# Performance work log

Measured on AMD Instinct MI355X. Metric: run time of the kernel, lower is better.

Reference implementation:

```python
import jax, jax.numpy as jnp
import numpy as np

D = 384      # n_embed_dims
H = 6        # n_heads
HS = D // H  # head_size = 64
T = 256      # block_size
B = 256
EPS = 1e-5


def setup_inputs() -> dict:
    key = jax.random.key(0)
    ks = jax.random.split(key, 12)
    s_in = 1.0 / np.sqrt(D)
    s_ff = 1.0 / np.sqrt(4 * D)
    return {
        "x": jax.random.normal(ks[0], (B, T, D), jnp.float32),
        # per-head QKV weights, stacked [H, D, HS] (Linear bias=False)
        "wq": jax.random.normal(ks[1], (H, D, HS), jnp.float32) * s_in,
        "wk": jax.random.normal(ks[2], (H, D, HS), jnp.float32) * s_in,
        "wv": jax.random.normal(ks[3], (H, D, HS), jnp.float32) * s_in,
        "w_proj": jax.random.normal(ks[4], (D, D), jnp.float32) * s_in,
        "b_proj": jax.random.normal(ks[5], (D,), jnp.float32) * s_in,
        "w1": jax.random.normal(ks[6], (D, 4 * D), jnp.float32) * s_in,
        "b1": jax.random.normal(ks[7], (4 * D,), jnp.float32) * s_in,
        "w2": jax.random.normal(ks[8], (4 * D, D), jnp.float32) * s_ff,
        "b2": jax.random.normal(ks[9], (D,), jnp.float32) * s_ff,
        "g1": jnp.ones((D,), jnp.float32),
        "be1": jnp.zeros((D,), jnp.float32),
        "g2": jnp.ones((D,), jnp.float32),
        "be2": jnp.zeros((D,), jnp.float32),
    }


def _layernorm(x, g, b):
    mu = jnp.mean(x, axis=-1, keepdims=True)
    var = jnp.mean(jnp.square(x - mu), axis=-1, keepdims=True)
    return (x - mu) * jax.lax.rsqrt(var + EPS) * g + b


def _attention(x, wq, wk, wv, w_proj, b_proj):
    # faithful quirk: scale = 1/sqrt(C) with C = full embed dim (384)
    scale = 1.0 / jnp.sqrt(jnp.asarray(D, x.dtype))
    q = jnp.einsum("btd,hde->bhte", x, wq)  # [B,H,T,HS]
    k = jnp.einsum("btd,hde->bhte", x, wk)
    v = jnp.einsum("btd,hde->bhte", x, wv)
    w = jnp.einsum("bhte,bhse->bhts", q, k) * scale  # [B,H,T,T], no mask
    w = jax.nn.softmax(w, axis=-1)
    out = jnp.einsum("bhts,bhse->bhte", w, v)  # [B,H,T,HS]
    # concat heads along feature dim (head order matches torch cat)
    out = out.transpose(0, 2, 1, 3).reshape(x.shape[0], x.shape[1], D)
    return out @ w_proj + b_proj


def reference(x, wq, wk, wv, w_proj, b_proj, w1, b1, w2, b2, g1, be1, g2, be2):
    x = x + _attention(_layernorm(x, g1, be1), wq, wk, wv, w_proj, b_proj)
    h = _layernorm(x, g2, be2)
    h = jax.nn.relu(h @ w1 + b1) @ w2 + b2  # dropout = eval-mode identity
    return x + h
```

## Files before the change

kernel.cpp:

```cpp
#include <hip/hip_runtime.h>
#include <stdint.h>

#define NTOK 65536
#define DE 384
#define QSTR 1280

typedef __bf16 bf16x8 __attribute__((ext_vector_type(8)));
typedef float  f32x4 __attribute__((ext_vector_type(4)));
typedef unsigned short u16x8 __attribute__((ext_vector_type(8)));

__device__ __forceinline__ unsigned short f2bf(float f) {
  union { float fl; unsigned u; } a; a.fl = f;
  unsigned r = a.u + 0x7fffu + ((a.u >> 16) & 1u);
  return (unsigned short)(r >> 16);
}

__device__ __forceinline__ void gll16(const void* g, void* l) {
  __builtin_amdgcn_global_load_lds((const __attribute__((address_space(1))) void*)g,
                                   (__attribute__((address_space(3))) void*)l, 16, 0, 0);
}

__device__ __forceinline__ bf16x8 ds128(unsigned addr) {
  bf16x8 r;
  asm volatile("ds_read_b128 %0, %1" : "=v"(r) : "v"(addr));
  return r;
}

__global__ void pack_t(unsigned short* __restrict__ dst, const float* __restrict__ src,
                       int R, int C) {
  int t = blockIdx.x * 256 + threadIdx.x;
  if (t >= R * C) return;
  int r = t / C, c = t - r * C;
  dst[(size_t)c * R + r] = f2bf(src[t]);
}

__global__ void qkv_pack(const float* __restrict__ wq, const float* __restrict__ wk,
                         const float* __restrict__ wv, unsigned short* __restrict__ dst) {
  int t = blockIdx.x * 256 + threadIdx.x;
  if (t >= QSTR * 384) return;
  int n = t / 384, k = t - n * 384;
  unsigned short v = 0;
  if (n < 1152) {
    int which = n / 384, r = n - which * 384;
    const float* src = which == 0 ? wq : (which == 1 ? wk : wv);
    int h = r >> 6, e = r & 63;
    v = f2bf(src[h * 24576 + k * 64 + e]);
  }
  dst[t] = v;
}

__global__ __launch_bounds__(256) void ln_kernel(const float* __restrict__ x,
                                                 const float* __restrict__ g,
                                                 const float* __restrict__ be,
                                                 unsigned short* __restrict__ out) {
  int wave = threadIdx.x >> 6, lane = threadIdx.x & 63;
  size_t row = (size_t)blockIdx.x * 4 + wave;
  const float* xr = x + row * DE;
  int c0 = lane * 2;
  float2 v0 = *(const float2*)(xr + c0);
  float2 v1 = *(const float2*)(xr + 128 + c0);
  float2 v2 = *(const float2*)(xr + 256 + c0);
  float s  = v0.x + v0.y + v1.x + v1.y + v2.x + v2.y;
  float ss = v0.x*v0.x + v0.y*v0.y + v1.x*v1.x + v1.y*v1.y + v2.x*v2.x + v2.y*v2.y;
#pragma unroll
  for (int m = 1; m < 64; m <<= 1) { s += __shfl_xor(s, m); ss += __shfl_xor(ss, m); }
  float mu = s * (1.0f / 384.0f);
  float rstd = rsqrtf(ss * (1.0f / 384.0f) - mu * mu + 1e-5f);
  unsigned short* orow = out + row * DE;
  {
    float a0 = (v0.x - mu) * rstd * g[c0] + be[c0];
    float a1 = (v0.y - mu) * rstd * g[c0 + 1] + be[c0 + 1];
    *(unsigned*)(orow + c0) = (unsigned)f2bf(a0) | ((unsigned)f2bf(a1) << 16);
  }
  {
    int c = c0 + 128;
    float a0 = (v1.x - mu) * rstd * g[c] + be[c];
    float a1 = (v1.y - mu) * rstd * g[c + 1] + be[c + 1];
    *(unsigned*)(orow + c) = (unsigned)f2bf(a0) | ((unsigned)f2bf(a1) << 16);
  }
  {
    int c = c0 + 256;
    float a0 = (v2.x - mu) * rstd * g[c] + be[c];
    float a1 = (v2.y - mu) * rstd * g[c + 1] + be[c + 1];
    *(unsigned*)(orow + c) = (unsigned)f2bf(a0) | ((unsigned)f2bf(a1) << 16);
  }
}

template<int EPI>
__device__ __forceinline__
void gemm_core(const unsigned short* __restrict__ A, const unsigned short* __restrict__ Bt,
               int M, int N, int K, int ntx,
               const float* __restrict__ bias, const float* __restrict__ resid,
               float* __restrict__ outf, unsigned short* __restrict__ outb) {
  __shared__ __align__(16) unsigned short As[2][4096];
  __shared__ __align__(16) unsigned short Bs[2][4096];
  const int tid = threadIdx.x;
  const int wave = tid >> 6, lane = tid & 63;

  const int nwg = gridDim.x;
  const int cpx = nwg >> 3;
  const int wg = (blockIdx.x & 7) * cpx + (blockIdx.x >> 3);
  const int bx = wg % ntx, by = wg / ntx;
  const int mBase = by << 7, nBase = bx << 7;
  const int wm = (wave >> 1) << 6, wn = (wave & 1) << 6;
  const int fr = lane & 15, fg = lane >> 4;

  const unsigned asb = (unsigned)(uintptr_t)&As[0][0];
  const unsigned bsb = (unsigned)(uintptr_t)&Bs[0][0];

  f32x4 acc[4][4];
  const f32x4 z = {0.f, 0.f, 0.f, 0.f};
#pragma unroll
  for (int i = 0; i < 4; ++i)
#pragma unroll
    for (int j = 0; j < 4; ++j) acc[i][j] = z;

  auto stage = [&](int buf, int kt) {
#pragma unroll
    for (int i = 0; i < 2; ++i) {
      int Lb = i * 4096 + wave * 1024;
      int L = Lb + lane * 16;
      int p = L >> 7;
      int sl = ((L >> 4) & 7) ^ (p & 7);
      int m = (p << 1) | (sl >> 2);
      int col = (sl & 3) << 3;
      gll16(A + (size_t)(mBase + m) * K + kt + col, (unsigned short*)As[buf] + (Lb >> 1));
      gll16(Bt + (size_t)(nBase + m) * K + kt + col, (unsigned short*)Bs[buf] + (Lb >> 1));
    }
  };

  auto fraddr = [&](unsigned base, int row) -> unsigned {
    return base + ((unsigned)(row >> 1) << 7) +
           ((unsigned)((fg | ((row & 1) << 2)) ^ ((row >> 1) & 7)) << 4);
  };

  const int NK = K >> 5;
  stage(0, 0);
  for (int t = 0; t < NK; ++t) {
    const int cur = t & 1;
    if (t + 1 < NK) {
      stage(cur ^ 1, (t + 1) << 5);
      asm volatile("s_waitcnt vmcnt(4)" ::: "memory");
    } else {
      asm volatile("s_waitcnt vmcnt(0)" ::: "memory");
    }
    asm volatile("" ::: "memory");
    __builtin_amdgcn_s_barrier();
    asm volatile("" ::: "memory");

    const unsigned ab = asb + (cur ? 8192u : 0u);
    const unsigned bb = bsb + (cur ? 8192u : 0u);
    bf16x8 af[4], bfr[4];
#pragma unroll
    for (int nb = 0; nb < 4; ++nb) bfr[nb] = ds128(fraddr(bb, wn + nb * 16 + fr));
#pragma unroll
    for (int mb = 0; mb < 4; ++mb) af[mb] = ds128(fraddr(ab, wm + mb * 16 + fr));
    asm volatile("s_waitcnt lgkmcnt(0)" ::: "memory");
    __builtin_amdgcn_sched_barrier(0);
    __builtin_amdgcn_s_setprio(1);
#pragma unroll
    for (int mb = 0; mb < 4; ++mb)
#pragma unroll
      for (int nb = 0; nb < 4; ++nb)
        acc[mb][nb] = __builtin_amdgcn_mfma_f32_16x16x32_bf16(af[mb], bfr[nb], acc[mb][nb], 0, 0, 0);
    __builtin_amdgcn_s_setprio(0);
    asm volatile("" ::: "memory");
    __builtin_amdgcn_s_barrier();
    asm volatile("" ::: "memory");
  }

#pragma unroll
  for (int mb = 0; mb < 4; ++mb) {
#pragma unroll
    for (int nb = 0; nb < 4; ++nb) {
      const int gn = nBase + wn + nb * 16 + fr;
#pragma unroll
      for (int i = 0; i < 4; ++i) {
        const int gm = mBase + wm + mb * 16 + (fg << 2) + i;
        float val = acc[mb][nb][i];
        if (EPI == 0) {
          outb[(size_t)gm * N + gn] = f2bf(val);
        } else if (EPI == 1) {
          size_t idx = (size_t)gm * N + gn;
          outf[idx] = val + bias[gn] + resid[idx];
        } else if (EPI == 2) {
          float r = val + bias[gn];
          outb[(size_t)gm * N + gn] = f2bf(r > 0.f ? r : 0.f);
        } else {
          size_t idx = (size_t)gm * N + gn;
          outf[idx] = val + bias[gn] + resid[idx];
        }
      }
    }
  }
}

__global__ __launch_bounds__(256, 4)
void gemm_qkv(const unsigned short* __restrict__ A, const unsigned short* __restrict__ Bt,
              int M, int N, int K, int ntx, const float* __restrict__ bias,
              const float* __restrict__ resid, float* __restrict__ outf,
              unsigned short* __restrict__ outb) {
  gemm_core<0>(A, Bt, M, N, K, ntx, bias, resid, outf, outb);
}
__global__ __launch_bounds__(256, 4)
void gemm_proj(const unsigned short* __restrict__ A, const unsigned short* __restrict__ Bt,
               int M, int N, int K, int ntx, const float* __restrict__ bias,
               const float* __restrict__ resid, float* __restrict__ outf,
               unsigned short* __restrict__ outb) {
  gemm_core<1>(A, Bt, M, N, K, ntx, bias, resid, outf, outb);
}
__global__ __launch_bounds__(256, 4)
void gemm_mlp1(const unsigned short* __restrict__ A, const unsigned short* __restrict__ Bt,
               int M, int N, int K, int ntx, const float* __restrict__ bias,
               const float* __restrict__ resid, float* __restrict__ outf,
               unsigned short* __restrict__ outb) {
  gemm_core<2>(A, Bt, M, N, K, ntx, bias, resid, outf, outb);
}
__global__ __launch_bounds__(256, 4)
void gemm_mlp2(const unsigned short* __restrict__ A, const unsigned short* __restrict__ Bt,
               int M, int N, int K, int ntx, const float* __restrict__ bias,
               const float* __restrict__ resid, float* __restrict__ outf,
               unsigned short* __restrict__ outb) {
  gemm_core<3>(A, Bt, M, N, K, ntx, bias, resid, outf, outb);
}

__global__ __launch_bounds__(256)
void attn_kernel(const unsigned short* __restrict__ qkvn, unsigned short* __restrict__ o) {
  __shared__ unsigned short Vt[64 * 256];
  __shared__ unsigned short Pw[4][64 * 32];
  const int bh = blockIdx.x;
  const int b = bh / 6, h = bh - b * 6;
  const unsigned short* base = qkvn + (size_t)(b * 256) * QSTR;
  const unsigned short* qb = base + h * 64;
  const unsigned short* kbp = base + 384 + h * 64;
  const unsigned short* vbp = base + 768 + h * 64;
  const int wave = threadIdx.x >> 6, lane = threadIdx.x & 63;
  const int fr = lane & 15, fg = lane >> 4;
  const int fk = fg << 3;
  const int qrow0 = wave << 6;
  const float scale = 0.051031036307982884f;
  const f32x4 z = {0.f, 0.f, 0.f, 0.f};

  {
    const int s = threadIdx.x;
    u16x8 v8[8];
#pragma unroll
    for (int j = 0; j < 8; ++j)
      v8[j] = *(const u16x8*)(vbp + (size_t)s * QSTR + j * 8);
#pragma unroll
    for (int e = 0; e < 64; ++e)
      Vt[(e << 8) + (s ^ ((e & 7) << 3))] = v8[e >> 3][e & 7];
  }
  __syncthreads();

  bf16x8 qf[4][2];
#pragma unroll
  for (int rb = 0; rb < 4; ++rb)
#pragma unroll
    for (int ks = 0; ks < 2; ++ks)
      qf[rb][ks] = *(const bf16x8*)(qb + (size_t)(qrow0 + rb * 16 + fr) * QSTR + ks * 32 + fk);

  float pm[4][4];
#pragma unroll
  for (int rb = 0; rb < 4; ++rb)
#pragma unroll
    for (int i = 0; i < 4; ++i) pm[rb][i] = -1e30f;

  for (int cb = 0; cb < 16; ++cb) {
    bf16x8 kf0 = *(const bf16x8*)(kbp + (size_t)(cb * 16 + fr) * QSTR + fk);
    bf16x8 kf1 = *(const bf16x8*)(kbp + (size_t)(cb * 16 + fr) * QSTR + 32 + fk);
#pragma unroll
    for (int rb = 0; rb < 4; ++rb) {
      f32x4 s = __builtin_amdgcn_mfma_f32_16x16x32_bf16(qf[rb][0], kf0, z, 0, 0, 0);
      s = __builtin_amdgcn_mfma_f32_16x16x32_bf16(qf[rb][1], kf1, s, 0, 0, 0);
#pragma unroll
      for (int i = 0; i < 4; ++i) pm[rb][i] = fmaxf(pm[rb][i], s[i]);
    }
  }
#pragma unroll
  for (int rb = 0; rb < 4; ++rb)
#pragma unroll
    for (int i = 0; i < 4; ++i) {
      float v = pm[rb][i];
      v = fmaxf(v, __shfl_xor(v, 1));
      v = fmaxf(v, __shfl_xor(v, 2));
      v = fmaxf(v, __shfl_xor(v, 4));
      v = fmaxf(v, __shfl_xor(v, 8));
      pm[rb][i] = v;
    }

  f32x4 oacc[4][4];
  float psum[4][4];
#pragma unroll
  for (int rb = 0; rb < 4; ++rb)
#pragma unroll
    for (int nb = 0; nb < 4; ++nb) oacc[rb][nb] = z;
#pragma unroll
  for (int rb = 0; rb < 4; ++rb)
#pragma unroll
    for (int i = 0; i < 4; ++i) psum[rb][i] = 0.f;

  for (int kb2 = 0; kb2 < 8; ++kb2) {
#pragma unroll
    for (int c2 = 0; c2 < 2; ++c2) {
      int cb = kb2 * 2 + c2;
      bf16x8 kf0 = *(const bf16x8*)(kbp + (size_t)(cb * 16 + fr) * QSTR + fk);
      bf16x8 kf1 = *(const bf16x8*)(kbp + (size_t)(cb * 16 + fr) * QSTR + 32 + fk);
#pragma unroll
      for (int rb = 0; rb < 4; ++rb) {
        f32x4 s = __builtin_amdgcn_mfma_f32_16x16x32_bf16(qf[rb][0], kf0, z, 0, 0, 0);
        s = __builtin_amdgcn_mfma_f32_16x16x32_bf16(qf[rb][1], kf1, s, 0, 0, 0);
#pragma unroll
        for (int i = 0; i < 4; ++i) {
          float p = __expf(scale * (s[i] - pm[rb][i]));
          psum[rb][i] += p;
          Pw[wave][(rb * 16 + (fg << 2) + i) * 32 + c2 * 16 + fr] = f2bf(p);
        }
      }
    }
    bf16x8 pa[4], vf[4];
#pragma unroll
    for (int rb = 0; rb < 4; ++rb) pa[rb] = *(const bf16x8*)(&Pw[wave][(rb * 16 + fr) * 32 + fk]);
#pragma unroll
    for (int nb = 0; nb < 4; ++nb) {
      int e = nb * 16 + fr;
      vf[nb] = *(const bf16x8*)(&Vt[(e << 8) + ((kb2 * 32 + fk) ^ ((e & 7) << 3))]);
    }
#pragma unroll
    for (int rb = 0; rb < 4; ++rb)
#pragma unroll
      for (int nb = 0; nb < 4; ++nb)
        oacc[rb][nb] = __builtin_amdgcn_mfma_f32_16x16x32_bf16(pa[rb], vf[nb], oacc[rb][nb], 0, 0, 0);
  }

  float rs[4][4];
#pragma unroll
  for (int rb = 0; rb < 4; ++rb)
#pragma unroll
    for (int i = 0; i < 4; ++i) {
      float v = psum[rb][i];
      v += __shfl_xor(v, 1);
      v += __shfl_xor(v, 2);
      v += __shfl_xor(v, 4);
      v += __shfl_xor(v, 8);
      rs[rb][i] = 1.0f / v;
    }

#pragma unroll
  for (int rb = 0; rb < 4; ++rb)
#pragma unroll
    for (int nb = 0; nb < 4; ++nb)
#pragma unroll
      for (int i = 0; i < 4; ++i) {
        int token = b * 256 + qrow0 + rb * 16 + (fg << 2) + i;
        int gcol = h * 64 + nb * 16 + fr;
        o[(size_t)token * DE + gcol] = f2bf(oacc[rb][nb][i] * rs[rb][i]);
      }
}

extern "C" void kernel_launch(void* const* d_in, const int* in_sizes, int n_in,
                              void* d_out, int out_size, void* d_ws, size_t ws_size,
                              hipStream_t stream) {
  const float* x     = (const float*)d_in[0];
  const float* wq    = (const float*)d_in[1];
  const float* wk    = (const float*)d_in[2];
  const float* wv    = (const float*)d_in[3];
  const float* wproj = (const float*)d_in[4];
  const float* bproj = (const float*)d_in[5];
  const float* w1    = (const float*)d_in[6];
  const float* b1    = (const float*)d_in[7];
  const float* w2    = (const float*)d_in[8];
  const float* b2    = (const float*)d_in[9];
  const float* g1    = (const float*)d_in[10];
  const float* be1   = (const float*)d_in[11];
  const float* g2    = (const float*)d_in[12];
  const float* be2   = (const float*)d_in[13];

  char* ws = (char*)d_ws;
  unsigned short* xln   = (unsigned short*)(ws + 0);
  float*          x1    = (float*)(ws + 0);
  unsigned short* qkvn  = (unsigned short*)(ws + 50331648);
  unsigned short* hbuf  = (unsigned short*)(ws + 100663296);
  unsigned short* act   = (unsigned short*)(ws + 150994944);
  unsigned short* attno = (unsigned short*)(ws + 218103808);
  unsigned short* wqkvt = (unsigned short*)(ws + 352321536);
  unsigned short* wprjt = (unsigned short*)(ws + 352321536 + 983040);
  unsigned short* w1t   = (unsigned short*)(ws + 352321536 + 983040 + 294912);
  unsigned short* w2t   = (unsigned short*)(ws + 352321536 + 983040 + 294912 + 1179648);

  qkv_pack<<<(QSTR * 384 + 255) / 256, 256, 0, stream>>>(wq, wk, wv, wqkvt);
  pack_t<<<(147456 + 255) / 256, 256, 0, stream>>>(wprjt, wproj, 384, 384);
  pack_t<<<(589824 + 255) / 256, 256, 0, stream>>>(w1t, w1, 384, 1536);
  pack_t<<<(589824 + 255) / 256, 256, 0, stream>>>(w2t, w2, 1536, 384);

  ln_kernel<<<NTOK / 4, 256, 0, stream>>>(x, g1, be1, xln);

  gemm_qkv<<<10 * 512, 256, 0, stream>>>(xln, wqkvt, NTOK, QSTR, 384, 10,
                                         nullptr, nullptr, nullptr, qkvn);

  attn_kernel<<<1536, 256, 0, stream>>>(qkvn, attno);

  gemm_proj<<<3 * 512, 256, 0, stream>>>(attno, wprjt, NTOK, 384, 384, 3,
                                         bproj, x, x1, nullptr);

  ln_kernel<<<NTOK / 4, 256, 0, stream>>>(x1, g2, be2, hbuf);

  gemm_mlp1<<<12 * 512, 256, 0, stream>>>(hbuf, w1t, NTOK, 1536, 384, 12,
                                          b1, nullptr, nullptr, act);

  gemm_mlp2<<<3 * 512, 256, 0, stream>>>(act, w2t, NTOK, 384, 1536, 3,
                                         b2, x1, (float*)d_out, nullptr);
}
```

Measured before the change: 575.3 us.

## Switch GEMMs to 256x256 tiles with 8 waves and 4-stage LDS pipeline

Replaces the 128x128, 4-wave GEMM core with a 256x256 tile computed by 8 waves (each 128x64), using a 4-buffer LDS ring with prefetch two k-steps ahead that is split into halves interleaved with the MFMA blocks. Larger tiles raise arithmetic intensity and cut global/LDS traffic per FLOP. For N=384 outputs the tile overhangs to 512, with padded weight buffers and a column guard in the epilogue, which wastes compute on those GEMMs. Occupancy drops to one 512-thread block per CU with 128KB LDS, and grid sizes fall (e.g. 512 blocks for proj/mlp2), which may leave CUs underused or cause tail effects.

```diff
diff --git a/kernel.cpp b/kernel.cpp
--- a/kernel.cpp
+++ b/kernel.cpp
@@ -88,12 +88,11 @@
 
 template<int EPI>
 __device__ __forceinline__
-void gemm_core(const unsigned short* __restrict__ A, const unsigned short* __restrict__ Bt,
-               int M, int N, int K, int ntx,
-               const float* __restrict__ bias, const float* __restrict__ resid,
-               float* __restrict__ outf, unsigned short* __restrict__ outb) {
-  __shared__ __align__(16) unsigned short As[2][4096];
-  __shared__ __align__(16) unsigned short Bs[2][4096];
+void gemm8_core(const unsigned short* __restrict__ A, const unsigned short* __restrict__ Bt,
+                int M, int Ncmp, int K, int Nout, int ntx,
+                const float* __restrict__ bias, const float* __restrict__ resid,
+                float* __restrict__ outf, unsigned short* __restrict__ outb) {
+  __shared__ __align__(16) unsigned short LB[4][16384];
   const int tid = threadIdx.x;
   const int wave = tid >> 6, lane = tid & 63;
 
@@ -101,60 +100,63 @@
   const int cpx = nwg >> 3;
   const int wg = (blockIdx.x & 7) * cpx + (blockIdx.x >> 3);
   const int bx = wg % ntx, by = wg / ntx;
-  const int mBase = by << 7, nBase = bx << 7;
-  const int wm = (wave >> 1) << 6, wn = (wave & 1) << 6;
+  const int mBase = by << 8, nBase = bx << 8;
+  const int wm = (wave >> 2) << 7, wn = (wave & 3) << 6;
   const int fr = lane & 15, fg = lane >> 4;
 
-  const unsigned asb = (unsigned)(uintptr_t)&As[0][0];
-  const unsigned bsb = (unsigned)(uintptr_t)&Bs[0][0];
-
-  f32x4 acc[4][4];
-  const f32x4 z = {0.f, 0.f, 0.f, 0.f};
-#pragma unroll
-  for (int i = 0; i < 4; ++i)
-#pragma unroll
-    for (int j = 0; j < 4; ++j) acc[i][j] = z;
-
-  auto stage = [&](int buf, int kt) {
-#pragma unroll
-    for (int i = 0; i < 2; ++i) {
-      int Lb = i * 4096 + wave * 1024;
-      int L = Lb + lane * 16;
-      int p = L >> 7;
-      int sl = ((L >> 4) & 7) ^ (p & 7);
-      int m = (p << 1) | (sl >> 2);
-      int col = (sl & 3) << 3;
-      gll16(A + (size_t)(mBase + m) * K + kt + col, (unsigned short*)As[buf] + (Lb >> 1));
-      gll16(Bt + (size_t)(nBase + m) * K + kt + col, (unsigned short*)Bs[buf] + (Lb >> 1));
-    }
+  unsigned short* lbase = &LB[0][0];
+  const unsigned asb = (unsigned)(uintptr_t)lbase;
+
+  const unsigned short* gsrc[4];
+  unsigned ldsoff[4];
+#pragma unroll
+  for (int c = 0; c < 4; ++c) {
+    int L = ((c & 1) << 13) + (wave << 10) + (lane << 4);
+    int p = L >> 7;
+    int sl = ((L >> 4) & 7) ^ (p & 7);
+    int m = (p << 1) | (sl >> 2);
+    int col = (sl & 3) << 3;
+    if (c < 2) gsrc[c] = A + (size_t)(mBase + m) * K + col;
+    else       gsrc[c] = Bt + (size_t)(nBase + m) * K + col;
+    ldsoff[c] = ((c < 2) ? (c << 12) : (8192 + ((c & 1) << 12))) + (wave << 9);
+  }
+  auto stage = [&](int b, int kt, int c) {
+    gll16(gsrc[c] + kt, lbase + b * 16384 + ldsoff[c]);
   };
-
-  auto fraddr = [&](unsigned base, int row) -> unsigned {
-    return base + ((unsigned)(row >> 1) << 7) +
+  auto fraddr = [&](unsigned rb, int row) -> unsigned {
+    return rb + ((unsigned)(row >> 1) << 7) +
            ((unsigned)((fg | ((row & 1) << 2)) ^ ((row >> 1) & 7)) << 4);
   };
 
+  f32x4 acc[8][4];
+  const f32x4 z = {0.f, 0.f, 0.f, 0.f};
+#pragma unroll
+  for (int i = 0; i < 8; ++i)
+#pragma unroll
+    for (int j = 0; j < 4; ++j) acc[i][j] = z;
+
   const int NK = K >> 5;
-  stage(0, 0);
+#pragma unroll
+  for (int c = 0; c < 4; ++c) stage(0, 0, c);
+#pragma unroll
+  for (int c = 0; c < 4; ++c) stage(1, 32, c);
+  asm volatile("s_waitcnt vmcnt(4)" ::: "memory");
+  __builtin_amdgcn_s_barrier();
+
   for (int t = 0; t < NK; ++t) {
-    const int cur = t & 1;
-    if (t + 1 < NK) {
-      stage(cur ^ 1, (t + 1) << 5);
-      asm volatile("s_waitcnt vmcnt(4)" ::: "memory");
-    } else {
-      asm volatile("s_waitcnt vmcnt(0)" ::: "memory");
-    }
-    asm volatile("" ::: "memory");
-    __builtin_amdgcn_s_barrier();
-    asm volatile("" ::: "memory");
-
-    const unsigned ab = asb + (cur ? 8192u : 0u);
-    const unsigned bb = bsb + (cur ? 8192u : 0u);
-    bf16x8 af[4], bfr[4];
+    const int b = t & 3;
+    const unsigned ab = asb + (unsigned)b * 32768u;
+    const unsigned bb = ab + 16384u;
+    const bool pf = (t + 2) < NK;
+    const int pb = (t + 2) & 3;
+    const int pkt = (t + 2) << 5;
+
+    bf16x8 bfr[4], af[4];
 #pragma unroll
     for (int nb = 0; nb < 4; ++nb) bfr[nb] = ds128(fraddr(bb, wn + nb * 16 + fr));
 #pragma unroll
     for (int mb = 0; mb < 4; ++mb) af[mb] = ds128(fraddr(ab, wm + mb * 16 + fr));
+    if (pf) { stage(pb, pkt, 0); stage(pb, pkt, 1); }
     asm volatile("s_waitcnt lgkmcnt(0)" ::: "memory");
     __builtin_amdgcn_sched_barrier(0);
     __builtin_amdgcn_s_setprio(1);
@@ -167,61 +169,82 @@
     asm volatile("" ::: "memory");
     __builtin_amdgcn_s_barrier();
     asm volatile("" ::: "memory");
-  }
-
-#pragma unroll
-  for (int mb = 0; mb < 4; ++mb) {
+
+#pragma unroll
+    for (int mb = 0; mb < 4; ++mb) af[mb] = ds128(fraddr(ab, wm + (4 + mb) * 16 + fr));
+    if (pf) { stage(pb, pkt, 2); stage(pb, pkt, 3); }
+    asm volatile("s_waitcnt lgkmcnt(0)" ::: "memory");
+    __builtin_amdgcn_sched_barrier(0);
+    __builtin_amdgcn_s_setprio(1);
+#pragma unroll
+    for (int mb = 0; mb < 4; ++mb)
+#pragma unroll
+      for (int nb = 0; nb < 4; ++nb)
+        acc[4 + mb][nb] = __builtin_amdgcn_mfma_f32_16x16x32_bf16(af[mb], bfr[nb], acc[4 + mb][nb], 0, 0, 0);
+    __builtin_amdgcn_s_setprio(0);
+    if (t + 1 < NK) {
+      if (t + 2 < NK) asm volatile("s_waitcnt vmcnt(4)" ::: "memory");
+      else            asm volatile("s_waitcnt vmcnt(0)" ::: "memory");
+      __builtin_amdgcn_s_barrier();
+      asm volatile("" ::: "memory");
+    }
+  }
+
+#pragma unroll
+  for (int mb = 0; mb < 8; ++mb) {
 #pragma unroll
     for (int nb = 0; nb < 4; ++nb) {
       const int gn = nBase + wn + nb * 16 + fr;
-#pragma unroll
-      for (int i = 0; i < 4; ++i) {
-        const int gm = mBase + wm + mb * 16 + (fg << 2) + i;
-        float val = acc[mb][nb][i];
-        if (EPI == 0) {
-          outb[(size_t)gm * N + gn] = f2bf(val);
-        } else if (EPI == 1) {
-          size_t idx = (size_t)gm * N + gn;
-          outf[idx] = val + bias[gn] + resid[idx];
-        } else if (EPI == 2) {
-          float r = val + bias[gn];
-          outb[(size_t)gm * N + gn] = f2bf(r > 0.f ? r : 0.f);
-        } else {
-          size_t idx = (size_t)gm * N + gn;
-          outf[idx] = val + bias[gn] + resid[idx];
+      if (gn < Nout) {
+#pragma unroll
+        for (int i = 0; i < 4; ++i) {
+          const int gm = mBase + wm + mb * 16 + (fg << 2) + i;
+          float val = acc[mb][nb][i];
+          if (EPI == 0) {
+            outb[(size_t)gm * Nout + gn] = f2bf(val);
+          } else if (EPI == 1) {
+            size_t idx = (size_t)gm * Nout + gn;
+            outf[idx] = val + bias[gn] + resid[idx];
+          } else if (EPI == 2) {
+            float r = val + bias[gn];
+            outb[(size_t)gm * Nout + gn] = f2bf(r > 0.f ? r : 0.f);
+          } else {
+            size_t idx = (size_t)gm * Nout + gn;
+            outf[idx] = val + bias[gn] + resid[idx];
+          }
         }
       }
     }
   }
 }
 
-__global__ __launch_bounds__(256, 4)
+__global__ __launch_bounds__(512, 1)
 void gemm_qkv(const unsigned short* __restrict__ A, const unsigned short* __restrict__ Bt,
-              int M, int N, int K, int ntx, const float* __restrict__ bias,
+              int M, int Ncmp, int K, int Nout, int ntx, const float* __restrict__ bias,
               const float* __restrict__ resid, float* __restrict__ outf,
               unsigned short* __restrict__ outb) {
-  gemm_core<0>(A, Bt, M, N, K, ntx, bias, resid, outf, outb);
-}
-__global__ __launch_bounds__(256, 4)
+  gemm8_core<0>(A, Bt, M, Ncmp, K, Nout, ntx, bias, resid, outf, outb);
+}
+__global__ __launch_bounds__(512, 1)
 void gemm_proj(const unsigned short* __restrict__ A, const unsigned short* __restrict__ Bt,
-               int M, int N, int K, int ntx, const float* __restrict__ bias,
+               int M, int Ncmp, int K, int Nout, int ntx, const float* __restrict__ bias,
                const float* __restrict__ resid, float* __restrict__ outf,
                unsigned short* __restrict__ outb) {
-  gemm_core<1>(A, Bt, M, N, K, ntx, bias, resid, outf, outb);
-}
-__global__ __launch_bounds__(256, 4)
+  gemm8_core<1>(A, Bt, M, Ncmp, K, Nout, ntx, bias, resid, outf, outb);
+}
+__global__ __launch_bounds__(512, 1)
 void gemm_mlp1(const unsigned short* __restrict__ A, const unsigned short* __restrict__ Bt,
-               int M, int N, int K, int ntx, const float* __restrict__ bias,
+               int M, int Ncmp, int K, int Nout, int ntx, const float* __restrict__ bias,
                const float* __restrict__ resid, float* __restrict__ outf,
                unsigned short* __restrict__ outb) {
-  gemm_core<2>(A, Bt, M, N, K, ntx, bias, resid, outf, outb);
-}
-__global__ __launch_bounds__(256, 4)
+  gemm8_core<2>(A, Bt, M, Ncmp, K, Nout, ntx, bias, resid, outf, outb);
+}
+__global__ __launch_bounds__(512, 1)
 void gemm_mlp2(const unsigned short* __restrict__ A, const unsigned short* __restrict__ Bt,
-               int M, int N, int K, int ntx, const float* __restrict__ bias,
+               int M, int Ncmp, int K, int Nout, int ntx, const float* __restrict__ bias,
                const float* __restrict__ resid, float* __restrict__ outf,
                unsigned short* __restrict__ outb) {
-  gemm_core<3>(A, Bt, M, N, K, ntx, bias, resid, outf, outb);
+  gemm8_core<3>(A, Bt, M, Ncmp, K, Nout, ntx, bias, resid, outf, outb);
 }
 
 __global__ __launch_bounds__(256)
@@ -385,8 +408,8 @@
   unsigned short* attno = (unsigned short*)(ws + 218103808);
   unsigned short* wqkvt = (unsigned short*)(ws + 352321536);
   unsigned short* wprjt = (unsigned short*)(ws + 352321536 + 983040);
-  unsigned short* w1t   = (unsigned short*)(ws + 352321536 + 983040 + 294912);
-  unsigned short* w2t   = (unsigned short*)(ws + 352321536 + 983040 + 294912 + 1179648);
+  unsigned short* w1t   = (unsigned short*)(ws + 352321536 + 983040 + 393216);
+  unsigned short* w2t   = (unsigned short*)(ws + 352321536 + 983040 + 393216 + 1179648);
 
   qkv_pack<<<(QSTR * 384 + 255) / 256, 256, 0, stream>>>(wq, wk, wv, wqkvt);
   pack_t<<<(147456 + 255) / 256, 256, 0, stream>>>(wprjt, wproj, 384, 384);
@@ -395,19 +418,19 @@
 
   ln_kernel<<<NTOK / 4, 256, 0, stream>>>(x, g1, be1, xln);
 
-  gemm_qkv<<<10 * 512, 256, 0, stream>>>(xln, wqkvt, NTOK, QSTR, 384, 10,
-                                         nullptr, nullptr, nullptr, qkvn);
+  gemm_qkv<<<5 * 256, 512, 0, stream>>>(xln, wqkvt, NTOK, 1280, 384, 1280, 5,
+                                        nullptr, nullptr, nullptr, qkvn);
 
   attn_kernel<<<1536, 256, 0, stream>>>(qkvn, attno);
 
-  gemm_proj<<<3 * 512, 256, 0, stream>>>(attno, wprjt, NTOK, 384, 384, 3,
+  gemm_proj<<<2 * 256, 512, 0, stream>>>(attno, wprjt, NTOK, 512, 384, 384, 2,
                                          bproj, x, x1, nullptr);
 
   ln_kernel<<<NTOK / 4, 256, 0, stream>>>(x1, g2, be2, hbuf);
 
-  gemm_mlp1<<<12 * 512, 256, 0, stream>>>(hbuf, w1t, NTOK, 1536, 384, 12,
-                                          b1, nullptr, nullptr, act);
-
-  gemm_mlp2<<<3 * 512, 256, 0, stream>>>(act, w2t, NTOK, 384, 1536, 3,
+  gemm_mlp1<<<6 * 256, 512, 0, stream>>>(hbuf, w1t, NTOK, 1536, 384, 1536, 6,
+                                         b1, nullptr, nullptr, act);
+
+  gemm_mlp2<<<2 * 256, 512, 0, stream>>>(act, w2t, NTOK, 512, 1536, 384, 2,
                                          b2, x1, (float*)d_out, nullptr);
 }
```

Result: slower. 618.3 us (+7.5%).
